# Optimization experiments

Measured on AMD Instinct MI355X. Metric: run time of the kernel, lower is better.

## Reference

```python
import jax, jax.numpy as jnp
import numpy as np

N_NODES = 100000
N_EDGES = 1600000
D_IN = 64
D_HID = 64
N_CLS = 4


def setup_inputs() -> dict:
    key = jax.random.key(0)
    ks = jax.random.split(key, 8)
    s = lambda d: 1.0 / np.sqrt(d)
    return {
        "node_features": jax.random.normal(ks[0], (N_NODES, D_IN), jnp.float32),
        "edge_src": jax.random.randint(ks[1], (N_EDGES,), 0, N_NODES, jnp.int32),
        "edge_dst": jax.random.randint(ks[2], (N_EDGES,), 0, N_NODES, jnp.int32),
        "W_self1": jax.random.normal(ks[3], (D_IN, D_HID), jnp.float32) * s(D_IN),
        "b_self1": jnp.zeros((D_HID,), jnp.float32),
        "W_neigh1": jax.random.normal(ks[4], (D_IN, D_HID), jnp.float32) * s(D_IN),
        "W_self2": jax.random.normal(ks[5], (D_HID, N_CLS), jnp.float32) * s(D_HID),
        "b_self2": jnp.zeros((N_CLS,), jnp.float32),
        "W_neigh2": jax.random.normal(ks[6], (D_HID, N_CLS), jnp.float32) * s(D_HID),
    }


def _sage_mean(h, edge_src, edge_dst, W_self, b_self, W_neigh, n_nodes):
    # mean aggregation over in-neighbors: gather src feats, segment-sum by dst
    msg_sum = jax.ops.segment_sum(h[edge_src], edge_dst, num_segments=n_nodes)
    deg = jax.ops.segment_sum(
        jnp.ones_like(edge_dst, dtype=h.dtype), edge_dst, num_segments=n_nodes
    )
    h_neigh = msg_sum / jnp.maximum(deg, 1.0)[:, None]
    # DGL SAGEConv: fc_self (with bias) + fc_neigh (no bias)
    return h @ W_self + b_self + h_neigh @ W_neigh


def reference(node_features, edge_src, edge_dst, W_self1, b_self1, W_neigh1,
              W_self2, b_self2, W_neigh2):
    n = node_features.shape[0]
    h1 = jnp.tanh(_sage_mean(node_features, edge_src, edge_dst,
                             W_self1, b_self1, W_neigh1, n))
    logits = _sage_mean(h1, edge_src, edge_dst, W_self2, b_self2, W_neigh2, n)
    return logits
```

## Files before the change

### kernel.cpp

```cpp
#include <hip/hip_runtime.h>
#include <hip/hip_bf16.h>
#include <stdint.h>

typedef unsigned char  u8;
typedef unsigned short u16;
typedef unsigned int   u32;
typedef __attribute__((ext_vector_type(8))) short bf16x8;
typedef __attribute__((ext_vector_type(2))) float f32x2;
typedef __attribute__((ext_vector_type(4))) float f32x4;
typedef __attribute__((ext_vector_type(4))) int   i32x4;

#define MAXB 256
#define BKT_SHIFT 9
#define BKT_NODES 512
#define CAP 12288
#define POISON 0xAAAAAAAAu
#define BINBLK 192
#define GEMMBLK 512

__device__ __forceinline__ float bf2f(u16 u) { return __uint_as_float(((u32)u) << 16); }
__device__ __forceinline__ u16 f2bf(float f) {
    u32 u = __float_as_uint(f);
    u += 0x7FFFu + ((u >> 16) & 1u);
    return (u16)(u >> 16);
}
__device__ __forceinline__ int pkbf(float a, float b) {
    return (int)__builtin_amdgcn_perm(__float_as_uint(b), __float_as_uint(a), 0x07060302u);
}
__device__ __forceinline__ u8 f2fp8(float v) {
    int p = __builtin_amdgcn_cvt_pk_fp8_f32(v, v, 0, false);
    return (u8)(p & 0xff);
}


__global__ __launch_bounds__(256) void k_front(const float* __restrict__ X,
                                               const float* __restrict__ Ws,
                                               const float* __restrict__ b1,
                                               const float* __restrict__ Wn,
                                               u16* __restrict__ Zb,
                                               u8* __restrict__ Y,
                                               int n,
                                               const int* __restrict__ src,
                                               const int* __restrict__ dst,
                                               u32* __restrict__ gcur,
                                               u32* __restrict__ binned,
                                               int E, int chunk, int nb) {
    __shared__ u16 wl[64 * 132];
    __shared__ int h[MAXB], base[MAXB], lcur[MAXB];
    int t = threadIdx.x;

    if ((int)blockIdx.x < BINBLK) {
        int blk = blockIdx.x;
        for (int i = t; i < nb; i += 256) h[i] = 0;
        __syncthreads();
        int beg = blk * chunk, end = min(beg + chunk, E);
        for (int i = beg + t; i < end; i += 256) atomicAdd(&h[dst[i] >> BKT_SHIFT], 1);
        __syncthreads();
        for (int i = t; i < nb; i += 256) {
            int c = h[i];
            base[i] = c ? (int)(atomicAdd(&gcur[i], (u32)c) - POISON) : 0;
            lcur[i] = 0;
        }
        __syncthreads();
        for (int i = beg + t; i < end; i += 256) {
            int d = dst[i], bk = d >> BKT_SHIFT;
            int p = base[bk] + atomicAdd(&lcur[bk], 1);
            if (p < CAP)
                binned[(size_t)bk * CAP + p] = ((u32)src[i] << BKT_SHIFT) | (u32)(d & (BKT_NODES - 1));
        }
        return;
    }

    for (int i = t; i < 8192; i += 256) {
        int k = i >> 7, c = i & 127;
        float w = (c < 64) ? Ws[k * 64 + c] : Wn[k * 64 + (c - 64)];
        wl[k * 132 + c] = f2bf(w);
    }
    __syncthreads();

    int wid = t >> 6, lane = t & 63;
    int lrow = lane & 15, lquad = lane >> 4;

    bf16x8 bfrag[8][2];
#pragma unroll
    for (int ct = 0; ct < 8; ct++)
#pragma unroll
        for (int kf = 0; kf < 2; kf++)
#pragma unroll
            for (int j = 0; j < 8; j++)
                bfrag[ct][kf][j] = (short)wl[(kf * 32 + lquad * 8 + j) * 132 + ct * 16 + lrow];

    float bias[4];
#pragma unroll
    for (int ct = 0; ct < 4; ct++) bias[ct] = b1[ct * 16 + lrow];

    int tiles = n >> 4;
    int tstride = GEMMBLK * 4;
    for (int tile = (blockIdx.x - BINBLK) * 4 + wid; tile < tiles; tile += tstride) {
        int nb4 = tile << 4;

        const float* xp = X + (size_t)(nb4 + lrow) * 64 + lquad * 8;
        f32x4 x0 = *(const f32x4*)(xp);
        f32x4 x1 = *(const f32x4*)(xp + 4);
        f32x4 x2 = *(const f32x4*)(xp + 32);
        f32x4 x3 = *(const f32x4*)(xp + 36);
        i32x4 p0, p1;
        p0.x = pkbf(x0.x, x0.y); p0.y = pkbf(x0.z, x0.w);
        p0.z = pkbf(x1.x, x1.y); p0.w = pkbf(x1.z, x1.w);
        p1.x = pkbf(x2.x, x2.y); p1.y = pkbf(x2.z, x2.w);
        p1.z = pkbf(x3.x, x3.y); p1.w = pkbf(x3.z, x3.w);
        bf16x8 af0 = __builtin_bit_cast(bf16x8, p0);
        bf16x8 af1 = __builtin_bit_cast(bf16x8, p1);

        f32x4 acc[8];
#pragma unroll
        for (int ct = 0; ct < 8; ct++) {
            f32x4 c = {0.f, 0.f, 0.f, 0.f};
            c = __builtin_amdgcn_mfma_f32_16x16x32_bf16(af0, bfrag[ct][0], c, 0, 0, 0);
            c = __builtin_amdgcn_mfma_f32_16x16x32_bf16(af1, bfrag[ct][1], c, 0, 0, 0);
            acc[ct] = c;
        }

        int rbase = nb4 + lquad * 4;
#pragma unroll
        for (int ct = 0; ct < 4; ct++)
#pragma unroll
            for (int r = 0; r < 4; r++)
                Zb[(size_t)(rbase + r) * 64 + ct * 16 + lrow] = f2bf(acc[ct][r] + bias[ct]);
#pragma unroll
        for (int ct = 0; ct < 4; ct++)
#pragma unroll
            for (int r = 0; r < 4; r++)
                Y[(size_t)(rbase + r) * 64 + ct * 16 + lrow] = f2fp8(acc[ct + 4][r]);
    }
}


__global__ __launch_bounds__(512) void k_csr(const u32* __restrict__ binned,
                                             const u32* __restrict__ gcur,
                                             int* __restrict__ rpb,
                                             int* __restrict__ rpe,
                                             int* __restrict__ col, int n) {
    __shared__ int cnt[BKT_NODES];
    __shared__ int wsum[8], woff[8];
    int b = blockIdx.x, t = threadIdx.x;
    int total = min((int)(gcur[b] - POISON), CAP);
    const u32* bb = binned + (size_t)b * CAP;
    cnt[t] = 0;
    __syncthreads();
    for (int i = t; i < total; i += 512)
        atomicAdd(&cnt[bb[i] & (BKT_NODES - 1)], 1);
    __syncthreads();
    int v = cnt[t];
    int lane = t & 63, w = t >> 6;
    int incl = v;
#pragma unroll
    for (int o = 1; o < 64; o <<= 1) {
        int x = __shfl_up(incl, o, 64);
        if (lane >= o) incl += x;
    }
    if (lane == 63) wsum[w] = incl;
    __syncthreads();
    if (t == 0) {
        int run = 0;
#pragma unroll
        for (int i = 0; i < 8; i++) { woff[i] = run; run += wsum[i]; }
    }
    __syncthreads();
    int excl = incl - v + woff[w];
    int gnode = b * BKT_NODES + t;
    int cb = b * CAP;
    if (gnode < n) { rpb[gnode] = cb + excl; rpe[gnode] = cb + excl + v; }
    cnt[t] = excl;
    __syncthreads();
    for (int i = t; i < total; i += 512) {
        u32 e = bb[i];
        int p = atomicAdd(&cnt[e & (BKT_NODES - 1)], 1);
        col[cb + p] = (int)(e >> BKT_SHIFT);
    }
}


__global__ __launch_bounds__(256) void k_gather1f(const int* __restrict__ rpb,
                                                  const int* __restrict__ rpe,
                                                  const int* __restrict__ col,
                                                  const u16* __restrict__ Zb,
                                                  const u8* __restrict__ Y,
                                                  const float* __restrict__ Ws2,
                                                  const float* __restrict__ b2,
                                                  const float* __restrict__ Wn2,
                                                  float* __restrict__ P,
                                                  u16* __restrict__ Q, int n) {
    int t = threadIdx.x;
    int q = t >> 4, l = t & 15;
    float wr[4][8], bb[4];
#pragma unroll
    for (int j = 0; j < 4; j++) {
        f32x4 a = *(const f32x4*)(Ws2 + (4 * l + j) * 4);
        f32x4 c = *(const f32x4*)(Wn2 + (4 * l + j) * 4);
        wr[j][0] = a.x; wr[j][1] = a.y; wr[j][2] = a.z; wr[j][3] = a.w;
        wr[j][4] = c.x; wr[j][5] = c.y; wr[j][6] = c.z; wr[j][7] = c.w;
    }
#pragma unroll
    for (int c = 0; c < 4; c++) bb[c] = b2[c];

    int node = blockIdx.x * 16 + q;
    if (node >= n) return;
    int beg = rpb[node], end = rpe[node];
    float a0 = 0.f, a1 = 0.f, a2 = 0.f, a3 = 0.f;
    int e = beg;
    for (; e + 4 <= end; e += 4) {
        int s0 = col[e], s1 = col[e + 1], s2 = col[e + 2], s3 = col[e + 3];
        u32 y0 = *(const u32*)(Y + (size_t)s0 * 64 + l * 4);
        u32 y1 = *(const u32*)(Y + (size_t)s1 * 64 + l * 4);
        u32 y2 = *(const u32*)(Y + (size_t)s2 * 64 + l * 4);
        u32 y3 = *(const u32*)(Y + (size_t)s3 * 64 + l * 4);
#pragma unroll
        for (int j = 0; j < 4; j++) {
            u32 yw = (j == 0) ? y0 : (j == 1) ? y1 : (j == 2) ? y2 : y3;
            f32x2 lo = __builtin_amdgcn_cvt_pk_f32_fp8(yw, false);
            f32x2 hi = __builtin_amdgcn_cvt_pk_f32_fp8(yw, true);
            a0 += lo.x; a1 += lo.y; a2 += hi.x; a3 += hi.y;
        }
    }
    for (; e < end; e++) {
        u32 yw = *(const u32*)(Y + (size_t)col[e] * 64 + l * 4);
        f32x2 lo = __builtin_amdgcn_cvt_pk_f32_fp8(yw, false);
        f32x2 hi = __builtin_amdgcn_cvt_pk_f32_fp8(yw, true);
        a0 += lo.x; a1 += lo.y; a2 += hi.x; a3 += hi.y;
    }
    float deg = (float)(end - beg);
    float inv = (deg > 0.f) ? 1.f / deg : 0.f;
    ushort4 z = *(const ushort4*)(Zb + (size_t)node * 64 + l * 4);
    float h0 = tanhf(bf2f(z.x) + a0 * inv);
    float h1 = tanhf(bf2f(z.y) + a1 * inv);
    float h2 = tanhf(bf2f(z.z) + a2 * inv);
    float h3 = tanhf(bf2f(z.w) + a3 * inv);

    float r[8];
#pragma unroll
    for (int c = 0; c < 8; c++)
        r[c] = h0 * wr[0][c] + h1 * wr[1][c] + h2 * wr[2][c] + h3 * wr[3][c];
#pragma unroll
    for (int m = 1; m < 16; m <<= 1)
#pragma unroll
        for (int c = 0; c < 8; c++) r[c] += __shfl_xor(r[c], m, 64);

    if (l == 0) {
        *(float4*)(P + (size_t)node * 4) =
            make_float4(r[0] + bb[0], r[1] + bb[1], r[2] + bb[2], r[3] + bb[3]);
        ushort4 qv;
        qv.x = f2bf(r[4]); qv.y = f2bf(r[5]); qv.z = f2bf(r[6]); qv.w = f2bf(r[7]);
        *(ushort4*)(Q + (size_t)node * 4) = qv;
    }
}


__global__ __launch_bounds__(256) void k_gather2(const int* __restrict__ rpb,
                                                 const int* __restrict__ rpe,
                                                 const int* __restrict__ col,
                                                 const float* __restrict__ P,
                                                 const u16* __restrict__ Q,
                                                 float* __restrict__ out, int n) {
    int node = blockIdx.x * 256 + threadIdx.x;
    if (node >= n) return;
    int beg = rpb[node], end = rpe[node];
    float a0 = 0.f, a1 = 0.f, a2 = 0.f, a3 = 0.f;
    int e = beg;
    for (; e + 4 <= end; e += 4) {
        int s0 = col[e], s1 = col[e + 1], s2 = col[e + 2], s3 = col[e + 3];
        ushort4 q0 = *(const ushort4*)(Q + (size_t)s0 * 4);
        ushort4 q1 = *(const ushort4*)(Q + (size_t)s1 * 4);
        ushort4 q2 = *(const ushort4*)(Q + (size_t)s2 * 4);
        ushort4 q3 = *(const ushort4*)(Q + (size_t)s3 * 4);
        a0 += bf2f(q0.x) + bf2f(q1.x) + bf2f(q2.x) + bf2f(q3.x);
        a1 += bf2f(q0.y) + bf2f(q1.y) + bf2f(q2.y) + bf2f(q3.y);
        a2 += bf2f(q0.z) + bf2f(q1.z) + bf2f(q2.z) + bf2f(q3.z);
        a3 += bf2f(q0.w) + bf2f(q1.w) + bf2f(q2.w) + bf2f(q3.w);
    }
    for (; e < end; e++) {
        ushort4 qv = *(const ushort4*)(Q + (size_t)col[e] * 4);
        a0 += bf2f(qv.x); a1 += bf2f(qv.y); a2 += bf2f(qv.z); a3 += bf2f(qv.w);
    }
    float deg = (float)(end - beg);
    float inv = (deg > 0.f) ? 1.f / deg : 0.f;
    float4 p = *(const float4*)(P + (size_t)node * 4);
    float4 o = make_float4(p.x + a0 * inv, p.y + a1 * inv,
                           p.z + a2 * inv, p.w + a3 * inv);
    *(float4*)(out + (size_t)node * 4) = o;
}


extern "C" void kernel_launch(void* const* d_in, const int* in_sizes, int n_in,
                              void* d_out, int out_size, void* d_ws, size_t ws_size,
                              hipStream_t stream) {
    const float* X   = (const float*)d_in[0];
    const int* esrc  = (const int*)d_in[1];
    const int* edst  = (const int*)d_in[2];
    const float* Ws1 = (const float*)d_in[3];
    const float* b1  = (const float*)d_in[4];
    const float* Wn1 = (const float*)d_in[5];
    const float* Ws2 = (const float*)d_in[6];
    const float* b2  = (const float*)d_in[7];
    const float* Wn2 = (const float*)d_in[8];
    float* out = (float*)d_out;

    const int n = in_sizes[0] / 64;
    const int E = in_sizes[1];
    const int nb = (n + BKT_NODES - 1) >> BKT_SHIFT;

    size_t off = 0;
    char* base = (char*)d_ws;
    auto give = [&](size_t bytes) -> char* {
        char* p = base + off;
        off += (bytes + 255) & ~(size_t)255;
        return p;
    };
    u32*   gcur   = (u32*)give((size_t)MAXB * 4);
    int*   rpb    = (int*)give((size_t)n * 4);
    int*   rpe    = (int*)give((size_t)n * 4);
    u32*   binned = (u32*)give((size_t)nb * CAP * 4);
    int*   col    = (int*)give((size_t)nb * CAP * 4);
    u16*   Zb     = (u16*)give((size_t)n * 64 * 2);
    u8*    Y      = (u8*)give((size_t)n * 64);
    float* P      = (float*)give((size_t)n * 4 * 4);
    u16*   Q      = (u16*)give((size_t)n * 4 * 2);

    const int chunk = (E + BINBLK - 1) / BINBLK;
    k_front<<<BINBLK + GEMMBLK, 256, 0, stream>>>(
        X, Ws1, b1, Wn1, Zb, Y, n,
        esrc, edst, gcur, binned, E, chunk, nb);

    k_csr<<<nb, 512, 0, stream>>>(binned, gcur, rpb, rpe, col, n);

    k_gather1f<<<(n + 15) / 16, 256, 0, stream>>>(rpb, rpe, col, Zb, Y,
                                                  Ws2, b2, Wn2, P, Q, n);
    k_gather2<<<(n + 255) / 256, 256, 0, stream>>>(rpb, rpe, col, P, Q, out, n);
}
```

Before: 184.5 us.

## Fuse CSR build into front kernel via grid-wide barrier among binning blocks

Removes the separate k_csr launch. The binning blocks now wait at a global atomic counter barrier, which relies on the POISON-initialised workspace, and then each builds the CSR for buckets strided by block index. It also doubles the GEMM block count so GEMM blocks overlap the CSR phase. This saves a kernel launch and lets the CSR work overlap the GEMM, at the risk of deadlock if not all 192 binning blocks are co-resident, and of fewer threads per bucket.

```diff
diff --git a/kernel.cpp b/kernel.cpp
--- a/kernel.cpp
+++ b/kernel.cpp
@@ -16,7 +16,7 @@
 #define CAP 12288
 #define POISON 0xAAAAAAAAu
 #define BINBLK 192
-#define GEMMBLK 512
+#define GEMMBLK 1024
 
 __device__ __forceinline__ float bf2f(u16 u) { return __uint_as_float(((u32)u) << 16); }
 __device__ __forceinline__ u16 f2bf(float f) {
@@ -43,10 +43,16 @@
                                                const int* __restrict__ src,
                                                const int* __restrict__ dst,
                                                u32* __restrict__ gcur,
+                                               u32* __restrict__ done,
                                                u32* __restrict__ binned,
+                                               int* __restrict__ rpb,
+                                               int* __restrict__ rpe,
+                                               int* __restrict__ col,
                                                int E, int chunk, int nb) {
     __shared__ u16 wl[64 * 132];
     __shared__ int h[MAXB], base[MAXB], lcur[MAXB];
+    __shared__ int cnt[BKT_NODES];
+    __shared__ int wsum[4], woff[4];
     int t = threadIdx.x;
 
     if ((int)blockIdx.x < BINBLK) {
@@ -67,6 +73,58 @@
             int p = base[bk] + atomicAdd(&lcur[bk], 1);
             if (p < CAP)
                 binned[(size_t)bk * CAP + p] = ((u32)src[i] << BKT_SHIFT) | (u32)(d & (BKT_NODES - 1));
+        }
+
+        __syncthreads();
+        if (t == 0) {
+            __threadfence();
+            __hip_atomic_fetch_add(done, 1u, __ATOMIC_ACQ_REL, __HIP_MEMORY_SCOPE_AGENT);
+            while (__hip_atomic_load(done, __ATOMIC_ACQUIRE, __HIP_MEMORY_SCOPE_AGENT)
+                   - POISON < (u32)BINBLK)
+                __builtin_amdgcn_s_sleep(8);
+            __threadfence();
+        }
+        __syncthreads();
+
+        int lane = t & 63, w = t >> 6;
+        for (int b = blk; b < nb; b += BINBLK) {
+            int total = min((int)(gcur[b] - POISON), CAP);
+            const u32* bb = binned + (size_t)b * CAP;
+            cnt[t] = 0; cnt[t + 256] = 0;
+            __syncthreads();
+            for (int i = t; i < total; i += 256)
+                atomicAdd(&cnt[bb[i] & (BKT_NODES - 1)], 1);
+            __syncthreads();
+            int c0 = cnt[2 * t], c1 = cnt[2 * t + 1];
+            int ps = c0 + c1;
+            int incl = ps;
+#pragma unroll
+            for (int o = 1; o < 64; o <<= 1) {
+                int x = __shfl_up(incl, o, 64);
+                if (lane >= o) incl += x;
+            }
+            if (lane == 63) wsum[w] = incl;
+            __syncthreads();
+            if (t == 0) {
+                int run = 0;
+#pragma unroll
+                for (int i = 0; i < 4; i++) { woff[i] = run; run += wsum[i]; }
+            }
+            __syncthreads();
+            int excl = incl - ps + woff[w];
+            int e0 = excl, e1 = excl + c0;
+            int gnode = b * BKT_NODES + 2 * t;
+            int cb = b * CAP;
+            if (gnode < n)     { rpb[gnode]     = cb + e0; rpe[gnode]     = cb + e0 + c0; }
+            if (gnode + 1 < n) { rpb[gnode + 1] = cb + e1; rpe[gnode + 1] = cb + e1 + c1; }
+            cnt[2 * t] = e0; cnt[2 * t + 1] = e1;
+            __syncthreads();
+            for (int i = t; i < total; i += 256) {
+                u32 e = bb[i];
+                int p = atomicAdd(&cnt[e & (BKT_NODES - 1)], 1);
+                col[cb + p] = (int)(e >> BKT_SHIFT);
+            }
+            __syncthreads();
         }
         return;
     }
@@ -132,51 +190,6 @@
 #pragma unroll
             for (int r = 0; r < 4; r++)
                 Y[(size_t)(rbase + r) * 64 + ct * 16 + lrow] = f2fp8(acc[ct + 4][r]);
-    }
-}
-
-
-__global__ __launch_bounds__(512) void k_csr(const u32* __restrict__ binned,
-                                             const u32* __restrict__ gcur,
-                                             int* __restrict__ rpb,
-                                             int* __restrict__ rpe,
-                                             int* __restrict__ col, int n) {
-    __shared__ int cnt[BKT_NODES];
-    __shared__ int wsum[8], woff[8];
-    int b = blockIdx.x, t = threadIdx.x;
-    int total = min((int)(gcur[b] - POISON), CAP);
-    const u32* bb = binned + (size_t)b * CAP;
-    cnt[t] = 0;
-    __syncthreads();
-    for (int i = t; i < total; i += 512)
-        atomicAdd(&cnt[bb[i] & (BKT_NODES - 1)], 1);
-    __syncthreads();
-    int v = cnt[t];
-    int lane = t & 63, w = t >> 6;
-    int incl = v;
-#pragma unroll
-    for (int o = 1; o < 64; o <<= 1) {
-        int x = __shfl_up(incl, o, 64);
-        if (lane >= o) incl += x;
-    }
-    if (lane == 63) wsum[w] = incl;
-    __syncthreads();
-    if (t == 0) {
-        int run = 0;
-#pragma unroll
-        for (int i = 0; i < 8; i++) { woff[i] = run; run += wsum[i]; }
-    }
-    __syncthreads();
-    int excl = incl - v + woff[w];
-    int gnode = b * BKT_NODES + t;
-    int cb = b * CAP;
-    if (gnode < n) { rpb[gnode] = cb + excl; rpe[gnode] = cb + excl + v; }
-    cnt[t] = excl;
-    __syncthreads();
-    for (int i = t; i < total; i += 512) {
-        u32 e = bb[i];
-        int p = atomicAdd(&cnt[e & (BKT_NODES - 1)], 1);
-        col[cb + p] = (int)(e >> BKT_SHIFT);
     }
 }
 
@@ -317,6 +330,7 @@
         return p;
     };
     u32*   gcur   = (u32*)give((size_t)MAXB * 4);
+    u32*   done   = (u32*)give(256);
     int*   rpb    = (int*)give((size_t)n * 4);
     int*   rpe    = (int*)give((size_t)n * 4);
     u32*   binned = (u32*)give((size_t)nb * CAP * 4);
@@ -329,9 +343,7 @@
     const int chunk = (E + BINBLK - 1) / BINBLK;
     k_front<<<BINBLK + GEMMBLK, 256, 0, stream>>>(
         X, Ws1, b1, Wn1, Zb, Y, n,
-        esrc, edst, gcur, binned, E, chunk, nb);
-
-    k_csr<<<nb, 512, 0, stream>>>(binned, gcur, rpb, rpe, col, n);
+        esrc, edst, gcur, done, binned, rpb, rpe, col, E, chunk, nb);
 
     k_gather1f<<<(n + 15) / 16, 256, 0, stream>>>(rpb, rpe, col, Zb, Y,
                                                   Ws2, b2, Wn2, P, Q, n);
```

New measurement: 235.8 us. 27.8% more time.

## Replace global-atomic edge binning with per-block local sort and offset table

Applied to the files above, without the earlier changes.

Edge binning no longer reserves space in global buckets through global atomics. Each binning block now sorts its chunk by bucket in shared memory, writes it out contiguously, and records per-bucket offsets in a table. The CSR kernel reads that table, gathers each bucket's segments from every binning block into shared memory, and sorts there before writing col in coalesced order. This removes global atomic contention and scattered writes, at the cost of more shared memory per block (which may lower occupancy) and an offset-table traversal across 256 blocks.

```diff
diff --git a/kernel.cpp b/kernel.cpp
--- a/kernel.cpp
+++ b/kernel.cpp
@@ -10,12 +10,10 @@
 typedef __attribute__((ext_vector_type(4))) float f32x4;
 typedef __attribute__((ext_vector_type(4))) int   i32x4;
 
-#define MAXB 256
 #define BKT_SHIFT 9
 #define BKT_NODES 512
 #define CAP 12288
-#define POISON 0xAAAAAAAAu
-#define BINBLK 192
+#define BINBLK 256
 #define GEMMBLK 512
 
 __device__ __forceinline__ float bf2f(u16 u) { return __uint_as_float(((u32)u) << 16); }
@@ -42,39 +40,61 @@
                                                int n,
                                                const int* __restrict__ src,
                                                const int* __restrict__ dst,
-                                               u32* __restrict__ gcur,
+                                               int* __restrict__ offT,
                                                u32* __restrict__ binned,
                                                int E, int chunk, int nb) {
-    __shared__ u16 wl[64 * 132];
-    __shared__ int h[MAXB], base[MAXB], lcur[MAXB];
+    __shared__ __align__(16) char sm[27264];
     int t = threadIdx.x;
 
     if ((int)blockIdx.x < BINBLK) {
+        u32* keys = (u32*)sm;
+        int* h    = (int*)(sm + 25600);
+        int* cur  = (int*)(sm + 26400);
+        int* ws4  = (int*)(sm + 27200);
         int blk = blockIdx.x;
+        int beg = blk * chunk, end = min(beg + chunk, E), m = max(0, end - beg);
+
         for (int i = t; i < nb; i += 256) h[i] = 0;
         __syncthreads();
-        int beg = blk * chunk, end = min(beg + chunk, E);
         for (int i = beg + t; i < end; i += 256) atomicAdd(&h[dst[i] >> BKT_SHIFT], 1);
         __syncthreads();
-        for (int i = t; i < nb; i += 256) {
-            int c = h[i];
-            base[i] = c ? (int)(atomicAdd(&gcur[i], (u32)c) - POISON) : 0;
-            lcur[i] = 0;
-        }
+        int v = (t < nb) ? h[t] : 0;
+        int lane = t & 63, w = t >> 6;
+        int incl = v;
+#pragma unroll
+        for (int o = 1; o < 64; o <<= 1) {
+            int x = __shfl_up(incl, o, 64);
+            if (lane >= o) incl += x;
+        }
+        if (lane == 63) ws4[w] = incl;
+        __syncthreads();
+        if (t == 0) {
+            int run = 0;
+#pragma unroll
+            for (int i = 0; i < 4; i++) { ws4[4 + i] = run; run += ws4[i]; }
+        }
+        __syncthreads();
+        int excl = incl - v + ws4[4 + w];
+        int* orow = offT + (size_t)blk * (nb + 1);
+        if (t < nb) { cur[t] = excl; orow[t] = excl; }
+        if (t == nb - 1) orow[nb] = excl + v;
         __syncthreads();
         for (int i = beg + t; i < end; i += 256) {
             int d = dst[i], bk = d >> BKT_SHIFT;
-            int p = base[bk] + atomicAdd(&lcur[bk], 1);
-            if (p < CAP)
-                binned[(size_t)bk * CAP + p] = ((u32)src[i] << BKT_SHIFT) | (u32)(d & (BKT_NODES - 1));
-        }
+            int p = atomicAdd(&cur[bk], 1);
+            keys[p] = ((u32)src[i] << BKT_SHIFT) | (u32)(d & (BKT_NODES - 1));
+        }
+        __syncthreads();
+        u32* outp = binned + (size_t)blk * chunk;
+        for (int i = t; i < m; i += 256) outp[i] = keys[i];
         return;
     }
 
+    u16* wl = (u16*)sm;
     for (int i = t; i < 8192; i += 256) {
         int k = i >> 7, c = i & 127;
-        float w = (c < 64) ? Ws[k * 64 + c] : Wn[k * 64 + (c - 64)];
-        wl[k * 132 + c] = f2bf(w);
+        float wv = (c < 64) ? Ws[k * 64 + c] : Wn[k * 64 + (c - 64)];
+        wl[k * 132 + c] = f2bf(wv);
     }
     __syncthreads();
 
@@ -137,22 +157,28 @@
 
 
 __global__ __launch_bounds__(512) void k_csr(const u32* __restrict__ binned,
-                                             const u32* __restrict__ gcur,
+                                             const int* __restrict__ offT,
                                              int* __restrict__ rpb,
                                              int* __restrict__ rpe,
-                                             int* __restrict__ col, int n) {
+                                             int* __restrict__ col,
+                                             int chunk, int nb, int n) {
+    __shared__ __align__(16) u32 ed[CAP];
+    __shared__ u32 srt[CAP];
+    __shared__ int gst[256], gln[256], soff[256];
     __shared__ int cnt[BKT_NODES];
     __shared__ int wsum[8], woff[8];
+    __shared__ int stot;
     int b = blockIdx.x, t = threadIdx.x;
-    int total = min((int)(gcur[b] - POISON), CAP);
-    const u32* bb = binned + (size_t)b * CAP;
-    cnt[t] = 0;
-    __syncthreads();
-    for (int i = t; i < total; i += 512)
-        atomicAdd(&cnt[bb[i] & (BKT_NODES - 1)], 1);
-    __syncthreads();
-    int v = cnt[t];
     int lane = t & 63, w = t >> 6;
+
+    if (t < 256) {
+        const int* row = offT + (size_t)t * (nb + 1);
+        int s = row[b], e = row[b + 1];
+        gst[t] = t * chunk + s;
+        gln[t] = e - s;
+    }
+    __syncthreads();
+    int v = (t < 256) ? gln[t] : 0;
     int incl = v;
 #pragma unroll
     for (int o = 1; o < 64; o <<= 1) {
@@ -165,19 +191,49 @@
         int run = 0;
 #pragma unroll
         for (int i = 0; i < 8; i++) { woff[i] = run; run += wsum[i]; }
-    }
-    __syncthreads();
-    int excl = incl - v + woff[w];
+        stot = run;
+    }
+    __syncthreads();
+    if (t < 256) soff[t] = incl - v + woff[w];
+    __syncthreads();
+    int total = min(stot, CAP);
+    for (int k = w; k < 256; k += 8) {
+        int g = gst[k], L = gln[k], o = soff[k];
+        for (int i = lane; i < L && o + i < CAP; i += 64) ed[o + i] = binned[g + i];
+    }
+    cnt[t] = 0;
+    __syncthreads();
+    for (int i = t; i < total; i += 512)
+        atomicAdd(&cnt[ed[i] & (BKT_NODES - 1)], 1);
+    __syncthreads();
+    int v2 = cnt[t];
+    int incl2 = v2;
+#pragma unroll
+    for (int o = 1; o < 64; o <<= 1) {
+        int x = __shfl_up(incl2, o, 64);
+        if (lane >= o) incl2 += x;
+    }
+    if (lane == 63) wsum[w] = incl2;
+    __syncthreads();
+    if (t == 0) {
+        int run = 0;
+#pragma unroll
+        for (int i = 0; i < 8; i++) { woff[i] = run; run += wsum[i]; }
+    }
+    __syncthreads();
+    int excl2 = incl2 - v2 + woff[w];
     int gnode = b * BKT_NODES + t;
     int cb = b * CAP;
-    if (gnode < n) { rpb[gnode] = cb + excl; rpe[gnode] = cb + excl + v; }
-    cnt[t] = excl;
+    if (gnode < n) { rpb[gnode] = cb + excl2; rpe[gnode] = cb + excl2 + v2; }
+    cnt[t] = excl2;
     __syncthreads();
     for (int i = t; i < total; i += 512) {
-        u32 e = bb[i];
+        u32 e = ed[i];
         int p = atomicAdd(&cnt[e & (BKT_NODES - 1)], 1);
-        col[cb + p] = (int)(e >> BKT_SHIFT);
-    }
+        srt[p] = e >> BKT_SHIFT;
+    }
+    __syncthreads();
+    for (int i = t; i < total; i += 512) col[cb + i] = (int)srt[i];
 }
 
 
@@ -308,6 +364,7 @@
     const int n = in_sizes[0] / 64;
     const int E = in_sizes[1];
     const int nb = (n + BKT_NODES - 1) >> BKT_SHIFT;
+    const int chunk = (E + BINBLK - 1) / BINBLK;
 
     size_t off = 0;
     char* base = (char*)d_ws;
@@ -316,22 +373,21 @@
         off += (bytes + 255) & ~(size_t)255;
         return p;
     };
-    u32*   gcur   = (u32*)give((size_t)MAXB * 4);
+    int*   offT   = (int*)give((size_t)BINBLK * (nb + 1) * 4);
     int*   rpb    = (int*)give((size_t)n * 4);
     int*   rpe    = (int*)give((size_t)n * 4);
-    u32*   binned = (u32*)give((size_t)nb * CAP * 4);
+    u32*   binned = (u32*)give((size_t)BINBLK * chunk * 4);
     int*   col    = (int*)give((size_t)nb * CAP * 4);
     u16*   Zb     = (u16*)give((size_t)n * 64 * 2);
     u8*    Y      = (u8*)give((size_t)n * 64);
     float* P      = (float*)give((size_t)n * 4 * 4);
     u16*   Q      = (u16*)give((size_t)n * 4 * 2);
 
-    const int chunk = (E + BINBLK - 1) / BINBLK;
     k_front<<<BINBLK + GEMMBLK, 256, 0, stream>>>(
         X, Ws1, b1, Wn1, Zb, Y, n,
-        esrc, edst, gcur, binned, E, chunk, nb);
-
-    k_csr<<<nb, 512, 0, stream>>>(binned, gcur, rpb, rpe, col, n);
+        esrc, edst, offT, binned, E, chunk, nb);
+
+    k_csr<<<nb, 512, 0, stream>>>(binned, offT, rpb, rpe, col, chunk, nb, n);
 
     k_gather1f<<<(n + 15) / 16, 256, 0, stream>>>(rpb, rpe, col, Zb, Y,
                                                   Ws2, b2, Wn2, P, Q, n);
```

Result: no change. 181.0 us (-1.9%).
